# Kernel tuning notes

Hardware: AMD Instinct MI355X
Metric: run time of the kernel (lower is better)

## Reference

```python
import jax, jax.numpy as jnp
import numpy as np


def setup_inputs() -> dict:
    key = jax.random.key(0)
    ks = jax.random.split(key, 8)
    B, C, H, W = 4, 96, 128, 128
    K, N, R = 2, 1, 6  # k_group directions, d_state, dt_rank=ceil(C/16)
    f = jax.random.normal
    return {
        "x": f(ks[0], (B, C, H, W), jnp.float32),
        "in_proj_w": f(ks[1], (2 * C, C), jnp.float32) * 0.05,   # 1x1 proj -> (x, z)
        "conv_w": f(ks[2], (C, 1, 3, 3), jnp.float32) * 0.1,     # depthwise 3x3
        "conv_b": f(ks[3], (C,), jnp.float32) * 0.02,
        "x_proj_w": f(ks[4], (K, R + 2 * N, C), jnp.float32) * 0.05,
        "dt_proj_w": jax.random.uniform(ks[5], (K, C, R), jnp.float32) * 0.1,  # initialize='v2'
        "dt_proj_b": jax.random.uniform(ks[6], (K, C), jnp.float32) * 0.1,
        "A_logs": jnp.zeros((K * C, N), jnp.float32),            # initialize='v2' -> A=-1
        "Ds": jnp.ones((K * C,), jnp.float32),
        "out_norm_w": jnp.ones((C,), jnp.float32),
        "out_norm_b": jnp.zeros((C,), jnp.float32),
        "out_proj_w": f(ks[7], (C, C), jnp.float32) * 0.05,
        "scale_w": jnp.ones((1, C, 1, 1), jnp.float32),          # _ScaleModule, init 1
    }


def reference(x, in_proj_w, conv_w, conv_b, x_proj_w, dt_proj_w, dt_proj_b,
              A_logs, Ds, out_norm_w, out_norm_b, out_proj_w, scale_w):
    B, C, H, W = x.shape
    K, N = dt_proj_w.shape[0], A_logs.shape[1]
    R = dt_proj_w.shape[2]
    L = H * W

    # in_proj (Linear2d, no bias) -> split into x and gate z
    xz = jnp.einsum('oc,bchw->bohw', in_proj_w, x)
    xc, z = xz[:, :C], xz[:, C:]

    # depthwise 3x3 conv + SiLU
    xc = jax.lax.conv_general_dilated(
        xc, conv_w, (1, 1), 'SAME',
        dimension_numbers=('NCHW', 'OIHW', 'NCHW'),
        feature_group_count=C) + conv_b[None, :, None, None]
    xc = jax.nn.silu(xc)

    # bidirectional cross-scan (k_group=2): row-major flatten and its reverse
    u = xc.reshape(B, C, L)
    xs = jnp.stack([u, u[:, :, ::-1]], axis=1)                    # (B,K,C,L)

    # input-dependent dt/B/C projections
    x_dbl = jnp.einsum('bkcl,kdc->bkdl', xs, x_proj_w)            # (B,K,R+2N,L)
    dts, Bs, Cs = x_dbl[:, :, :R], x_dbl[:, :, R:R + N], x_dbl[:, :, R + N:]
    delta = jax.nn.softplus(
        jnp.einsum('bkrl,kcr->bkcl', dts, dt_proj_w) + dt_proj_b[None, :, :, None])

    A = -jnp.exp(A_logs).reshape(K, C, N)
    dA = jnp.exp(delta[..., None] * A[None, :, :, None, :])       # (B,K,C,L,N)
    dBu = (delta * xs)[..., None] * jnp.swapaxes(Bs, -1, -2)[:, :, None]  # (B,K,C,L,N)

    def step(h, inp):
        dA_l, dBu_l, C_l = inp                                    # (B,K,C,N),(B,K,C,N),(B,K,N)
        h = dA_l * h + dBu_l
        y = jnp.einsum('bkcn,bkn->bkc', h, C_l)
        return h, y

    h0 = jnp.zeros((B, K, C, N), x.dtype)
    _, ys = jax.lax.scan(step, h0, (jnp.moveaxis(dA, 3, 0),
                                    jnp.moveaxis(dBu, 3, 0),
                                    jnp.moveaxis(Cs, 3, 0)))      # ys: (L,B,K,C)
    ys = jnp.moveaxis(ys, 0, 3) + Ds.reshape(K, C)[None, :, :, None] * xs  # (B,K,C,L)

    # cross-merge: un-flip reverse direction and sum
    y = (ys[:, 0] + ys[:, 1, :, ::-1]).reshape(B, C, H, W)

    # out_norm: LayerNorm2d over channels (channel_first)
    mu = y.mean(1, keepdims=True)
    var = y.var(1, keepdims=True)
    y = (y - mu) * jax.lax.rsqrt(var + 1e-5)
    y = y * out_norm_w[None, :, None, None] + out_norm_b[None, :, None, None]

    # gate and out_proj (Linear2d, no bias)
    y = y * jax.nn.silu(z)
    out = jnp.einsum('oc,bchw->bohw', out_proj_w, y)

    # base_scale (_ScaleModule); stride=1 so no do_stride
    return scale_w * out
```

## Files before the change

### kernel.cpp

```cpp
#include <hip/hip_runtime.h>
#include <hip/hip_fp16.h>
#include <math.h>

#define Bn 4
#define Cn 96
#define Hn 128
#define Wn 128
#define Ln (Hn*Wn)
#define Kn 2
#define Rn 6
#define SC 16
#define NCH (Ln/SC)

__device__ __forceinline__ float siluf(float x) { return x / (1.f + __expf(-x)); }
__device__ __forceinline__ float softplusf(float x) {
    return fmaxf(x, 0.f) + __logf(1.f + __expf(-fabsf(x)));
}

__global__ __launch_bounds__(256, 3) void k_inproj(
    const float* __restrict__ x, const float* __restrict__ ipw,
    float* __restrict__ xc, float* __restrict__ zs)
{
    __shared__ float smem[4096 + 6272];
    float* xls = smem;
    float* wls = smem + 4096;
    float* stage = smem;

    const int t  = threadIdx.x;
    const int b  = blockIdx.x >> 7;
    const int l0 = (blockIdx.x & 127) << 7;
    const int tx = t & 15;
    const int ty = t >> 4;

    float acc[12][8];
#pragma unroll
    for (int i = 0; i < 12; ++i)
#pragma unroll
        for (int j = 0; j < 8; ++j) acc[i][j] = 0.f;

    const float* xbase = x + (size_t)b * Cn * Ln + l0;

    for (int k0 = 0; k0 < Cn; k0 += 32) {
        if (k0) __syncthreads();
        {
            int idx = t;
#pragma unroll
            for (int q = 0; q < 4; ++q, idx += 256) {
                int k = idx >> 5, p4 = idx & 31;
                *(float4*)&xls[k * 128 + p4 * 4] =
                    *(const float4*)&xbase[(size_t)(k0 + k) * Ln + p4 * 4];
            }
        }
        for (int idx = t; idx < 32 * 192; idx += 256) {
            int o = idx % 192, k = idx / 192;
            wls[k * 196 + o] = ipw[o * Cn + k0 + k];
        }
        __syncthreads();

#pragma unroll 2
        for (int kk = 0; kk < 32; ++kk) {
            float4 xv0 = *(const float4*)&xls[kk * 128 + tx * 4];
            float4 xv1 = *(const float4*)&xls[kk * 128 + 64 + tx * 4];
            const float* wrow = &wls[kk * 196 + ty * 12];
            float4 w0 = *(const float4*)&wrow[0];
            float4 w1 = *(const float4*)&wrow[4];
            float4 w2 = *(const float4*)&wrow[8];
            float wv[12] = {w0.x,w0.y,w0.z,w0.w,w1.x,w1.y,w1.z,w1.w,w2.x,w2.y,w2.z,w2.w};
            float xa[8]  = {xv0.x,xv0.y,xv0.z,xv0.w,xv1.x,xv1.y,xv1.z,xv1.w};
#pragma unroll
            for (int i = 0; i < 12; ++i)
#pragma unroll
                for (int j = 0; j < 8; ++j)
                    acc[i][j] = fmaf(wv[i], xa[j], acc[i][j]);
        }
    }

    const size_t tilebase = (size_t)b * Ln + l0;
#pragma unroll
    for (int half_ = 0; half_ < 2; ++half_) {
        __syncthreads();
        if (ty < 8) {
#pragma unroll
            for (int j = 0; j < 4; ++j)
#pragma unroll
                for (int i = 0; i < 12; ++i)
                    stage[(tx * 4 + j) * 100 + ty * 12 + i] = acc[i][half_ * 4 + j];
        }
        __syncthreads();
        {
            float4* dst = (float4*)(xc + (tilebase + half_ * 64) * Cn);
            for (int idx = t; idx < 1536; idx += 256) {
                int p = idx / 24, c4 = idx % 24;
                dst[idx] = *(const float4*)&stage[p * 100 + c4 * 4];
            }
        }
        __syncthreads();
        if (ty >= 8) {
#pragma unroll
            for (int j = 0; j < 4; ++j)
#pragma unroll
                for (int i = 0; i < 12; ++i)
                    stage[(tx * 4 + j) * 100 + (ty - 8) * 12 + i] = siluf(acc[i][half_ * 4 + j]);
        }
        __syncthreads();
        {
            float4* dst = (float4*)(zs + (tilebase + half_ * 64) * Cn);
            for (int idx = t; idx < 1536; idx += 256) {
                int p = idx / 24, c4 = idx % 24;
                dst[idx] = *(const float4*)&stage[p * 100 + c4 * 4];
            }
        }
    }
}

__global__ __launch_bounds__(256) void k_conv(
    const float* __restrict__ xc, const float* __restrict__ cw,
    const float* __restrict__ cb, float* __restrict__ u)
{
    const int e   = blockIdx.x * 256 + threadIdx.x;
    const int c   = e % Cn;
    const int pos = e / Cn;
    const int l   = pos % Ln;
    const int b   = pos / Ln;
    const int h   = l >> 7, w = l & 127;

    float acc = cb[c];
#pragma unroll
    for (int dh = -1; dh <= 1; ++dh) {
        int hh = h + dh;
        if (hh < 0 || hh >= Hn) continue;
#pragma unroll
        for (int dw = -1; dw <= 1; ++dw) {
            int ww = w + dw;
            if (ww < 0 || ww >= Wn) continue;
            acc = fmaf(cw[c*9 + (dh+1)*3 + (dw+1)],
                       xc[((size_t)b * Ln + (hh << 7) + ww) * Cn + c], acc);
        }
    }
    u[e] = siluf(acc);
}

__global__ __launch_bounds__(768) void k_part1(
    const float* __restrict__ u, const float* __restrict__ xpw,
    const float* __restrict__ dtw, const float* __restrict__ dtb,
    const float* __restrict__ Alogs, const float* __restrict__ Ds,
    float* __restrict__ Pc, float* __restrict__ Qc,
    float* __restrict__ y0, __half* __restrict__ f)
{
    __shared__ float uls[64 * 100];
    __shared__ float xd[64 * 16];
    __shared__ float yt[64 * 104];
    __shared__ float dsum[96];
    const int t  = threadIdx.x;
    const int j  = blockIdx.x & 255;
    const int b  = blockIdx.x >> 8;
    const int l0 = j << 6;

    {
        const float4* up4 = (const float4*)(u + ((size_t)b * Ln + l0) * Cn);
        for (int e4 = t; e4 < 1536; e4 += 768) {
            int p = e4 / 24, c4 = e4 % 24;
            *(float4*)&uls[p * 100 + c4 * 4] = up4[e4];
        }
    }
    if (t < 96) dsum[t] = Ds[t] + Ds[Cn + t];
    __syncthreads();

    for (int dp = t; dp < 1024; dp += 768) {
        int dd = dp & 15, p = dp >> 4;
        const float4* wr = (const float4*)(xpw + dd * Cn);
        const float4* ur = (const float4*)&uls[p * 100];
        float acc = 0.f;
#pragma unroll
        for (int c4 = 0; c4 < 24; ++c4) {
            float4 w = wr[c4], v = ur[c4];
            acc = fmaf(w.x, v.x, acc); acc = fmaf(w.y, v.y, acc);
            acc = fmaf(w.z, v.z, acc); acc = fmaf(w.w, v.w, acc);
        }
        xd[p * 16 + dd] = acc;
    }
    __syncthreads();

    const int c  = t % 96;
    const int ci = (t / 96) & 3;
    const int k  = t / 384;
    const int bk = b * Kn + k;
    const float Av = -__expf(Alogs[k * Cn + c]);
    const float bias = dtb[k * Cn + c];
    float dtwr[Rn];
#pragma unroll
    for (int r = 0; r < Rn; ++r) dtwr[r] = dtw[(k * Cn + c) * Rn + r];

    const int chunk = (k == 0) ? (4 * j + ci) : (1020 - 4 * j + ci);
    const int xoff = k * 8;
    __half* fkc = f + ((size_t)(b * Ln + l0) * 2 + k) * Cn + c;

    float h = 0.f, cp = 1.f;
    float yreg[SC];
#pragma unroll
    for (int hf = 0; hf < 2; ++hf) {
        float dAv[8], dBu[8], Cl[8];
#pragma unroll
        for (int i = 0; i < 8; ++i) {
            const int ii = hf * 8 + i;
            const int p = (k == 0) ? (ci * 16 + ii) : ((3 - ci) * 16 + (15 - ii));
            const float* xr = &xd[p * 16 + xoff];
            float de = bias;
#pragma unroll
            for (int r = 0; r < Rn; ++r) de = fmaf(dtwr[r], xr[r], de);
            de = softplusf(de);
            dAv[i] = __expf(de * Av);
            dBu[i] = de * uls[p * 100 + c] * xr[6];
            Cl[i]  = xr[7];
        }
#pragma unroll
        for (int i = 0; i < 8; ++i) {
            const int ii = hf * 8 + i;
            const int p = (k == 0) ? (ci * 16 + ii) : ((3 - ci) * 16 + (15 - ii));
            h  = fmaf(dAv[i], h, dBu[i]);
            cp *= dAv[i];
            yreg[ii] = h * Cl[i];
            fkc[(size_t)p * (2 * Cn)] = __float2half(cp * Cl[i]);
        }
    }
    {
        const size_t cidx = ((size_t)bk * NCH + chunk) * Cn + c;
        Pc[cidx] = cp;
        Qc[cidx] = h;
    }

    if (k == 0) {
#pragma unroll
        for (int i = 0; i < SC; ++i) {
            int p = ci * 16 + i;
            yt[p * 104 + c] = yreg[i] + dsum[c] * uls[p * 100 + c];
        }
    }
    __syncthreads();
    if (k == 1) {
#pragma unroll
        for (int i = 0; i < SC; ++i) {
            int p = (3 - ci) * 16 + (15 - i);
            yt[p * 104 + c] += yreg[i];
        }
    }
    __syncthreads();
    {
        float4* y4 = (float4*)(y0 + ((size_t)b * Ln + l0) * Cn);
        for (int e4 = t; e4 < 1536; e4 += 768) {
            int p = e4 / 24, c4 = e4 % 24;
            y4[e4] = *(const float4*)&yt[p * 104 + c4 * 4];
        }
    }
}

__global__ __launch_bounds__(1024) void k_scan2(
    const float* __restrict__ Pc, const float* __restrict__ Qc,
    float* __restrict__ hinit)
{
    __shared__ float Pg[32][33], Qg[32][33], gini[32][33];
    const int bk    = blockIdx.x / 3;
    const int cbase = (blockIdx.x % 3) * 32;
    const int t = threadIdx.x;
    const int c = t & 31, g = t >> 5;

    const size_t base = ((size_t)bk * NCH + g * 32) * Cn + cbase + c;
    float P = 1.f, Q = 0.f;
    for (int j = 0; j < 32; ++j) {
        size_t idx = base + (size_t)j * Cn;
        float p_ = Pc[idx], q_ = Qc[idx];
        Q = fmaf(p_, Q, q_);
        P *= p_;
    }
    Pg[g][c] = P; Qg[g][c] = Q;
    __syncthreads();
    if (t < 32) {
        float h = 0.f;
        for (int gg = 0; gg < 32; ++gg) {
            gini[gg][t] = h;
            h = fmaf(Pg[gg][t], h, Qg[gg][t]);
        }
    }
    __syncthreads();
    float h = gini[g][c];
    for (int j = 0; j < 32; ++j) {
        size_t idx = base + (size_t)j * Cn;
        hinit[idx] = h;
        h = fmaf(Pc[idx], h, Qc[idx]);
    }
}

__global__ __launch_bounds__(512) void k_merge(
    const float* __restrict__ y0, const __half* __restrict__ f,
    const float* __restrict__ hinit, const float* __restrict__ zs,
    const float* __restrict__ onw, const float* __restrict__ onb,
    const float* __restrict__ opw, const float* __restrict__ scw,
    float* __restrict__ out)
{
    __shared__ float gt[64 * 104];
    __shared__ float wls[96 * 36];
    __shared__ float h0s[4 * 96], h1s[4 * 96];
    __shared__ float mu[64], isd[64];
    const int t  = threadIdx.x;
    const int j  = blockIdx.x & 255;
    const int b  = blockIdx.x >> 8;
    const int l0 = j << 6;

    for (int idx = t; idx < 768; idx += 512) {
        if (idx < 384) {
            int q = idx / 96, c = idx % 96;
            h0s[q * 96 + c] = hinit[((size_t)(b * 2 + 0) * NCH + 4 * j + q) * Cn + c];
        } else {
            int i2 = idx - 384;
            int q = i2 / 96, c = i2 % 96;
            h1s[q * 96 + c] = hinit[((size_t)(b * 2 + 1) * NCH + (1023 - 4 * j - q)) * Cn + c];
        }
    }
    __syncthreads();

    {
        const float4* y4 = (const float4*)(y0 + ((size_t)b * Ln + l0) * Cn);
        const __half* fb = f + (size_t)(b * Ln + l0) * 2 * Cn;
        for (int e4 = t; e4 < 1536; e4 += 512) {
            int p = e4 / 24, c4 = e4 % 24;
            float4 yv = y4[e4];
            const __half* fp0 = fb + (size_t)p * (2 * Cn) + c4 * 4;
            const __half2* f0h = (const __half2*)fp0;
            const __half2* f1h = (const __half2*)(fp0 + Cn);
            float2 fa0 = __half22float2(f0h[0]);
            float2 fa1 = __half22float2(f0h[1]);
            float2 fb0 = __half22float2(f1h[0]);
            float2 fb1 = __half22float2(f1h[1]);
            const float4 h0v = *(const float4*)&h0s[(p >> 4) * 96 + c4 * 4];
            const float4 h1v = *(const float4*)&h1s[(p >> 4) * 96 + c4 * 4];
            yv.x = fmaf(h0v.x, fa0.x, fmaf(h1v.x, fb0.x, yv.x));
            yv.y = fmaf(h0v.y, fa0.y, fmaf(h1v.y, fb0.y, yv.y));
            yv.z = fmaf(h0v.z, fa1.x, fmaf(h1v.z, fb1.x, yv.z));
            yv.w = fmaf(h0v.w, fa1.y, fmaf(h1v.w, fb1.y, yv.w));
            *(float4*)&gt[p * 104 + c4 * 4] = yv;
        }
    }
    __syncthreads();

    if (t < 256) {
        const int p = t >> 2, q = t & 3;
        const float4* row = (const float4*)&gt[p * 104 + q * 24];
        float s = 0.f, ss = 0.f;
#pragma unroll
        for (int i = 0; i < 6; ++i) {
            float4 v = row[i];
            s  += v.x + v.y + v.z + v.w;
            ss += v.x*v.x + v.y*v.y + v.z*v.z + v.w*v.w;
        }
        s  += __shfl_xor(s, 1);  s  += __shfl_xor(s, 2);
        ss += __shfl_xor(ss, 1); ss += __shfl_xor(ss, 2);
        if (q == 0) {
            float m = s * (1.f / Cn);
            mu[p] = m;
            isd[p] = rsqrtf(ss * (1.f / Cn) - m * m + 1e-5f);
        }
    }
    __syncthreads();

    {
        const float4* zp4 = (const float4*)(zs + ((size_t)b * Ln + l0) * Cn);
        const float4* w4  = (const float4*)onw;
        const float4* b4  = (const float4*)onb;
        for (int e4 = t; e4 < 1536; e4 += 512) {
            int p = e4 / 24, c4 = e4 % 24;
            float4 v = *(const float4*)&gt[p * 104 + c4 * 4];
            float4 wv = w4[c4], bv = b4[c4], zv = zp4[e4];
            float m = mu[p], is = isd[p];
            v.x = ((v.x - m) * is * wv.x + bv.x) * zv.x;
            v.y = ((v.y - m) * is * wv.y + bv.y) * zv.y;
            v.z = ((v.z - m) * is * wv.z + bv.z) * zv.z;
            v.w = ((v.w - m) * is * wv.w + bv.w) * zv.w;
            *(float4*)&gt[p * 104 + c4 * 4] = v;
        }
    }

    const int og = t & 31, pg = t >> 5;
    float acc[3][4];
#pragma unroll
    for (int i = 0; i < 3; ++i)
#pragma unroll
        for (int r = 0; r < 4; ++r) acc[i][r] = 0.f;

    for (int k0 = 0; k0 < Cn; k0 += 32) {
        __syncthreads();
        for (int e4 = t; e4 < 768; e4 += 512) {
            int o = e4 >> 3, c4 = e4 & 7;
            *(float4*)&wls[o * 36 + c4 * 4] = *(const float4*)&opw[o * Cn + k0 + c4 * 4];
        }
        __syncthreads();
#pragma unroll
        for (int c4 = 0; c4 < 8; ++c4) {
            float4 w0 = *(const float4*)&wls[(og * 3 + 0) * 36 + c4 * 4];
            float4 w1 = *(const float4*)&wls[(og * 3 + 1) * 36 + c4 * 4];
            float4 w2 = *(const float4*)&wls[(og * 3 + 2) * 36 + c4 * 4];
            float4 g0 = *(const float4*)&gt[(pg * 4 + 0) * 104 + k0 + c4 * 4];
            float4 g1 = *(const float4*)&gt[(pg * 4 + 1) * 104 + k0 + c4 * 4];
            float4 g2 = *(const float4*)&gt[(pg * 4 + 2) * 104 + k0 + c4 * 4];
            float4 g3 = *(const float4*)&gt[(pg * 4 + 3) * 104 + k0 + c4 * 4];
#define ACC1(i, wv, r, gv) \
            acc[i][r] = fmaf(wv.x, gv.x, acc[i][r]); \
            acc[i][r] = fmaf(wv.y, gv.y, acc[i][r]); \
            acc[i][r] = fmaf(wv.z, gv.z, acc[i][r]); \
            acc[i][r] = fmaf(wv.w, gv.w, acc[i][r]);
            ACC1(0, w0, 0, g0) ACC1(0, w0, 1, g1) ACC1(0, w0, 2, g2) ACC1(0, w0, 3, g3)
            ACC1(1, w1, 0, g0) ACC1(1, w1, 1, g1) ACC1(1, w1, 2, g2) ACC1(1, w1, 3, g3)
            ACC1(2, w2, 0, g0) ACC1(2, w2, 1, g1) ACC1(2, w2, 2, g2) ACC1(2, w2, 3, g3)
#undef ACC1
        }
    }

    __syncthreads();
#pragma unroll
    for (int i = 0; i < 3; ++i)
#pragma unroll
        for (int r = 0; r < 4; ++r)
            gt[(og * 3 + i) * 68 + pg * 4 + r] = acc[i][r];
    __syncthreads();

    {
        float* ob = out + (size_t)b * Cn * Ln + l0;
        for (int e4 = t; e4 < 1536; e4 += 512) {
            int o = e4 >> 4, p4 = e4 & 15;
            float4 v = *(const float4*)&gt[o * 68 + p4 * 4];
            float sc = scw[o];
            v.x *= sc; v.y *= sc; v.z *= sc; v.w *= sc;
            *(float4*)&ob[(size_t)o * Ln + p4 * 4] = v;
        }
    }
}

extern "C" void kernel_launch(void* const* d_in, const int* in_sizes, int n_in,
                              void* d_out, int out_size, void* d_ws, size_t ws_size,
                              hipStream_t stream)
{
    const float* x     = (const float*)d_in[0];
    const float* ipw   = (const float*)d_in[1];
    const float* cw    = (const float*)d_in[2];
    const float* cb    = (const float*)d_in[3];
    const float* xpw   = (const float*)d_in[4];
    const float* dtw   = (const float*)d_in[5];
    const float* dtb   = (const float*)d_in[6];
    const float* Alogs = (const float*)d_in[7];
    const float* Ds    = (const float*)d_in[8];
    const float* onw   = (const float*)d_in[9];
    const float* onb   = (const float*)d_in[10];
    const float* opw   = (const float*)d_in[11];
    const float* scw   = (const float*)d_in[12];
    float* out = (float*)d_out;

    float* wsp = (float*)d_ws;
    size_t off = 0;
    float* xc   = wsp + off;
    float* y0   = wsp + off; off += (size_t)Bn * Ln * Cn;
    float* zs   = wsp + off; off += (size_t)Bn * Ln * Cn;
    float* u    = wsp + off; off += (size_t)Bn * Ln * Cn;
    __half* f   = (__half*)u;
    float* Pc    = wsp + off; off += (size_t)Bn * Kn * NCH * Cn;
    float* Qc    = wsp + off; off += (size_t)Bn * Kn * NCH * Cn;
    float* hinit = wsp + off; off += (size_t)Bn * Kn * NCH * Cn;

    k_inproj<<<Bn * 128, 256, 0, stream>>>(x, ipw, xc, zs);
    k_conv  <<<(Bn * Ln * Cn) / 256, 256, 0, stream>>>(xc, cw, cb, u);
    k_part1 <<<Bn * 256, 768, 0, stream>>>(u, xpw, dtw, dtb, Alogs, Ds,
                                           Pc, Qc, y0, f);
    k_scan2 <<<24, 1024, 0, stream>>>(Pc, Qc, hinit);
    k_merge <<<Bn * 256, 512, 0, stream>>>(y0, f, hinit, zs, onw, onb,
                                           opw, scw, out);
}
```

Measured before the change: 287.3 us.

## Vectorize depthwise conv to float4 and shrink part1 blocks with reused smem

The depthwise conv kernel now has each thread compute four channels using float4 loads, with the conv weights staged transposed in shared memory, which cuts the thread count and load instructions by four. k_part1 is reworked to handle 32 positions per block with 384 threads instead of 64 with 768. It drops the separate yt buffer by writing y back into uls, and folds the D-skip term into the scan loop. This lowers shared-memory use to raise occupancy, at the cost of more blocks and an extra barrier.

```diff
diff --git a/kernel.cpp b/kernel.cpp
--- a/kernel.cpp
+++ b/kernel.cpp
@@ -117,14 +117,22 @@
     const float* __restrict__ xc, const float* __restrict__ cw,
     const float* __restrict__ cb, float* __restrict__ u)
 {
+    __shared__ float cws[9 * 96];
+    for (int i = threadIdx.x; i < 864; i += 256) {
+        int cc = i % 96, tap = i / 96;
+        cws[tap * 96 + cc] = cw[cc * 9 + tap];
+    }
+    __syncthreads();
+
     const int e   = blockIdx.x * 256 + threadIdx.x;
-    const int c   = e % Cn;
-    const int pos = e / Cn;
+    const int c4  = e % 24;
+    const int pos = e / 24;
     const int l   = pos % Ln;
     const int b   = pos / Ln;
     const int h   = l >> 7, w = l & 127;
-
-    float acc = cb[c];
+    const int c   = c4 * 4;
+
+    float4 acc = *(const float4*)&cb[c];
 #pragma unroll
     for (int dh = -1; dh <= 1; ++dh) {
         int hh = h + dh;
@@ -133,32 +141,37 @@
         for (int dw = -1; dw <= 1; ++dw) {
             int ww = w + dw;
             if (ww < 0 || ww >= Wn) continue;
-            acc = fmaf(cw[c*9 + (dh+1)*3 + (dw+1)],
-                       xc[((size_t)b * Ln + (hh << 7) + ww) * Cn + c], acc);
-        }
-    }
-    u[e] = siluf(acc);
-}
-
-__global__ __launch_bounds__(768) void k_part1(
+            float4 wv = *(const float4*)&cws[((dh + 1) * 3 + (dw + 1)) * 96 + c];
+            float4 xv = *(const float4*)&xc[((size_t)b * Ln + (hh << 7) + ww) * Cn + c];
+            acc.x = fmaf(wv.x, xv.x, acc.x);
+            acc.y = fmaf(wv.y, xv.y, acc.y);
+            acc.z = fmaf(wv.z, xv.z, acc.z);
+            acc.w = fmaf(wv.w, xv.w, acc.w);
+        }
+    }
+    float4 r;
+    r.x = siluf(acc.x); r.y = siluf(acc.y); r.z = siluf(acc.z); r.w = siluf(acc.w);
+    *(float4*)&u[((size_t)b * Ln + l) * Cn + c] = r;
+}
+
+__global__ __launch_bounds__(384, 8) void k_part1(
     const float* __restrict__ u, const float* __restrict__ xpw,
     const float* __restrict__ dtw, const float* __restrict__ dtb,
     const float* __restrict__ Alogs, const float* __restrict__ Ds,
     float* __restrict__ Pc, float* __restrict__ Qc,
     float* __restrict__ y0, __half* __restrict__ f)
 {
-    __shared__ float uls[64 * 100];
-    __shared__ float xd[64 * 16];
-    __shared__ float yt[64 * 104];
+    __shared__ float uls[32 * 100];
+    __shared__ float xd[32 * 16];
     __shared__ float dsum[96];
     const int t  = threadIdx.x;
-    const int j  = blockIdx.x & 255;
-    const int b  = blockIdx.x >> 8;
-    const int l0 = j << 6;
+    const int j  = blockIdx.x & 511;
+    const int b  = blockIdx.x >> 9;
+    const int l0 = j << 5;
 
     {
         const float4* up4 = (const float4*)(u + ((size_t)b * Ln + l0) * Cn);
-        for (int e4 = t; e4 < 1536; e4 += 768) {
+        for (int e4 = t; e4 < 768; e4 += 384) {
             int p = e4 / 24, c4 = e4 % 24;
             *(float4*)&uls[p * 100 + c4 * 4] = up4[e4];
         }
@@ -166,7 +179,7 @@
     if (t < 96) dsum[t] = Ds[t] + Ds[Cn + t];
     __syncthreads();
 
-    for (int dp = t; dp < 1024; dp += 768) {
+    for (int dp = t; dp < 512; dp += 384) {
         int dd = dp & 15, p = dp >> 4;
         const float4* wr = (const float4*)(xpw + dd * Cn);
         const float4* ur = (const float4*)&uls[p * 100];
@@ -182,16 +195,17 @@
     __syncthreads();
 
     const int c  = t % 96;
-    const int ci = (t / 96) & 3;
-    const int k  = t / 384;
+    const int ci = (t / 96) & 1;
+    const int k  = t / 192;
     const int bk = b * Kn + k;
     const float Av = -__expf(Alogs[k * Cn + c]);
     const float bias = dtb[k * Cn + c];
+    const float dsc = dsum[c];
     float dtwr[Rn];
 #pragma unroll
     for (int r = 0; r < Rn; ++r) dtwr[r] = dtw[(k * Cn + c) * Rn + r];
 
-    const int chunk = (k == 0) ? (4 * j + ci) : (1020 - 4 * j + ci);
+    const int chunk = (k == 0) ? (2 * j + ci) : (1022 - 2 * j + ci);
     const int xoff = k * 8;
     __half* fkc = f + ((size_t)(b * Ln + l0) * 2 + k) * Cn + c;
 
@@ -199,27 +213,28 @@
     float yreg[SC];
 #pragma unroll
     for (int hf = 0; hf < 2; ++hf) {
-        float dAv[8], dBu[8], Cl[8];
+        float dAv[8], dBu[8], Cl[8], uv[8];
 #pragma unroll
         for (int i = 0; i < 8; ++i) {
             const int ii = hf * 8 + i;
-            const int p = (k == 0) ? (ci * 16 + ii) : ((3 - ci) * 16 + (15 - ii));
+            const int p = (k == 0) ? (ci * 16 + ii) : ((1 - ci) * 16 + (15 - ii));
             const float* xr = &xd[p * 16 + xoff];
             float de = bias;
 #pragma unroll
             for (int r = 0; r < Rn; ++r) de = fmaf(dtwr[r], xr[r], de);
             de = softplusf(de);
+            uv[i]  = uls[p * 100 + c];
             dAv[i] = __expf(de * Av);
-            dBu[i] = de * uls[p * 100 + c] * xr[6];
+            dBu[i] = de * uv[i] * xr[6];
             Cl[i]  = xr[7];
         }
 #pragma unroll
         for (int i = 0; i < 8; ++i) {
             const int ii = hf * 8 + i;
-            const int p = (k == 0) ? (ci * 16 + ii) : ((3 - ci) * 16 + (15 - ii));
+            const int p = (k == 0) ? (ci * 16 + ii) : ((1 - ci) * 16 + (15 - ii));
             h  = fmaf(dAv[i], h, dBu[i]);
             cp *= dAv[i];
-            yreg[ii] = h * Cl[i];
+            yreg[ii] = (k == 0) ? fmaf(dsc, uv[i], h * Cl[i]) : (h * Cl[i]);
             fkc[(size_t)p * (2 * Cn)] = __float2half(cp * Cl[i]);
         }
     }
@@ -229,27 +244,28 @@
         Qc[cidx] = h;
     }
 
+    __syncthreads();
     if (k == 0) {
 #pragma unroll
         for (int i = 0; i < SC; ++i) {
             int p = ci * 16 + i;
-            yt[p * 104 + c] = yreg[i] + dsum[c] * uls[p * 100 + c];
+            uls[p * 100 + c] = yreg[i];
         }
     }
     __syncthreads();
     if (k == 1) {
 #pragma unroll
         for (int i = 0; i < SC; ++i) {
-            int p = (3 - ci) * 16 + (15 - i);
-            yt[p * 104 + c] += yreg[i];
+            int p = (1 - ci) * 16 + (15 - i);
+            uls[p * 100 + c] += yreg[i];
         }
     }
     __syncthreads();
     {
         float4* y4 = (float4*)(y0 + ((size_t)b * Ln + l0) * Cn);
-        for (int e4 = t; e4 < 1536; e4 += 768) {
+        for (int e4 = t; e4 < 768; e4 += 384) {
             int p = e4 / 24, c4 = e4 % 24;
-            y4[e4] = *(const float4*)&yt[p * 104 + c4 * 4];
+            y4[e4] = *(const float4*)&uls[p * 100 + c4 * 4];
         }
     }
 }
@@ -465,8 +481,8 @@
     float* hinit = wsp + off; off += (size_t)Bn * Kn * NCH * Cn;
 
     k_inproj<<<Bn * 128, 256, 0, stream>>>(x, ipw, xc, zs);
-    k_conv  <<<(Bn * Ln * Cn) / 256, 256, 0, stream>>>(xc, cw, cb, u);
-    k_part1 <<<Bn * 256, 768, 0, stream>>>(u, xpw, dtw, dtb, Alogs, Ds,
+    k_conv  <<<(Bn * Ln * 24) / 256, 256, 0, stream>>>(xc, cw, cb, u);
+    k_part1 <<<Bn * 512, 384, 0, stream>>>(u, xpw, dtw, dtb, Alogs, Ds,
                                            Pc, Qc, y0, f);
     k_scan2 <<<24, 1024, 0, stream>>>(Pc, Qc, hinit);
     k_merge <<<Bn * 256, 512, 0, stream>>>(y0, f, hinit, zs, onw, onb,
```

Result: slower. 298.1 us (+3.8%).
